# Optimization experiments

Hardware: AMD Instinct MI355X
Metric: run time of the kernel (lower is better)

The kernel has to match this reference:

```python
import jax, jax.numpy as jnp
import numpy as np

B, T, C, H = 2, 2048, 1024, 16
D = C // H  # head dim = 64

def setup_inputs() -> dict:
    key = jax.random.key(0)
    k1, k2, k3 = jax.random.split(key, 3)
    x = jax.random.normal(k1, (B, T, C), dtype=jnp.float32)
    w_attn = jax.random.normal(k2, (C, 3 * C), dtype=jnp.float32) * (1.0 / np.sqrt(C))
    w_proj = jax.random.normal(k3, (C, C), dtype=jnp.float32) * (1.0 / np.sqrt(C))
    return {"x": x, "w_attn": w_attn, "w_proj": w_proj}

def reference(x, w_attn, w_proj):
    # qkv projection: [B,T,3C]
    qkv = jnp.einsum('btc,cd->btd', x, w_attn)
    q, k, v = jnp.split(qkv, 3, axis=-1)
    # reshape to [B,H,T,D]
    q = q.reshape(B, T, H, D).transpose(0, 2, 1, 3)
    k = k.reshape(B, T, H, D).transpose(0, 2, 1, 3)
    v = v.reshape(B, T, H, D).transpose(0, 2, 1, 3)
    scale = 1.0 / jnp.sqrt(jnp.asarray(D, dtype=q.dtype))
    att = jnp.einsum('bhqd,bhkd->bhqk', q, k) * scale  # [B,H,T,T]
    att = jax.nn.softmax(att, axis=-1)
    y = jnp.einsum('bhqk,bhkd->bhqd', att, v)  # [B,H,T,D]
    y = y.transpose(0, 2, 1, 3).reshape(B, T, C)
    return jnp.einsum('btc,cd->btd', y, w_proj)
```

## Files before the change

kernel.cpp:

```cpp
#include <hip/hip_runtime.h>
#include <hip/hip_bf16.h>


typedef unsigned short u16;
using bf16x8 = __attribute__((ext_vector_type(8))) short;
using f32x4  = __attribute__((ext_vector_type(4))) float;

#define T_SEQ 2048
#define CDIM  1024

#define QSCALE 0.18033688011112042f

#if __has_builtin(__builtin_amdgcn_exp2f)
#define EXP2(x) __builtin_amdgcn_exp2f(x)
#else
#define EXP2(x) __expf((x) * 0.6931471805599453f)
#endif

__device__ inline u16 f2bf(float f) {
  __hip_bfloat16 h = __float2bfloat16(f);
  return *reinterpret_cast<u16*>(&h);
}

__device__ inline void gload_lds16(const u16* g, u16* l) {
  __builtin_amdgcn_global_load_lds((const __attribute__((address_space(1))) void*)g,
                                   (__attribute__((address_space(3))) void*)l, 16, 0, 0);
}

__device__ inline int swz128(int r, int c) {
  return (((r << 7) + (c << 1)) ^ ((r & 7) << 4)) >> 1;
}

__global__ __launch_bounds__(256) void conv_bf16_kernel(const float* __restrict__ in,
                                                        u16* __restrict__ out, int n4) {
  int idx = blockIdx.x * 256 + threadIdx.x;
  if (idx >= n4) return;
  float4 v = reinterpret_cast<const float4*>(in)[idx];
  ushort4 o;
  o.x = f2bf(v.x); o.y = f2bf(v.y); o.z = f2bf(v.z); o.w = f2bf(v.w);
  reinterpret_cast<ushort4*>(out)[idx] = o;
}

__global__ __launch_bounds__(256) void transp_conv_kernel(const float* __restrict__ in,
                                                          u16* __restrict__ out, int R, int N,
                                                          int scale_rows, float scale) {
  __shared__ float tile[32][33];
  int nbx = N >> 5;
  int bx = blockIdx.x % nbx, by = blockIdx.x / nbx;
  int tx = threadIdx.x & 31, ty = threadIdx.x >> 5;
#pragma unroll
  for (int rr = ty; rr < 32; rr += 8)
    tile[rr][tx] = in[(long)(by * 32 + rr) * N + bx * 32 + tx];
  __syncthreads();
#pragma unroll
  for (int rr = ty; rr < 32; rr += 8) {
    float s = (bx * 32 + rr) < scale_rows ? scale : 1.0f;
    out[(long)(bx * 32 + rr) * R + by * 32 + tx] = f2bf(tile[tx][rr] * s);
  }
}

template <bool OUT_F32>
__global__ __launch_bounds__(256) void gemm_bt_kernel(const u16* __restrict__ A,
                                                      const u16* __restrict__ Bt,
                                                      void* __restrict__ C,
                                                      int N, int K) {
  __shared__ u16 As[2][128 * 32];
  __shared__ u16 Bs[2][128 * 32];
  const int tid = threadIdx.x;
  const int lane = tid & 63, wid = tid >> 6;
  const int l16 = lane & 15, lh = lane >> 4;
  const int wm = wid >> 1, wn = wid & 1;
  const int tm = blockIdx.x & 31;
  const int tn = blockIdx.x >> 5;

  f32x4 acc[4][4];
#pragma unroll
  for (int i = 0; i < 4; ++i)
#pragma unroll
    for (int j = 0; j < 4; ++j)
      acc[i][j] = f32x4{0.f, 0.f, 0.f, 0.f};

  const long aRow = (long)(tm * 128 + wid * 16 + (lane >> 2)) * K + (lane & 3) * 8;
  const long bRow = (long)(tn * 128 + wid * 16 + (lane >> 2)) * K + (lane & 3) * 8;
  const long rstep = (long)64 * K;
  const int ldsOff = wid * 512;

  gload_lds16(A + aRow, As[0] + ldsOff);
  gload_lds16(A + aRow + rstep, As[0] + ldsOff + 2048);
  gload_lds16(Bt + bRow, Bs[0] + ldsOff);
  gload_lds16(Bt + bRow + rstep, Bs[0] + ldsOff + 2048);
  __syncthreads();

  int cur = 0;
  for (int k0 = 0; k0 < K; k0 += 32) {
    if (k0 + 32 < K) {
      gload_lds16(A + aRow + k0 + 32, As[cur ^ 1] + ldsOff);
      gload_lds16(A + aRow + rstep + k0 + 32, As[cur ^ 1] + ldsOff + 2048);
      gload_lds16(Bt + bRow + k0 + 32, Bs[cur ^ 1] + ldsOff);
      gload_lds16(Bt + bRow + rstep + k0 + 32, Bs[cur ^ 1] + ldsOff + 2048);
    }
    bf16x8 af[4], bfr[4];
#pragma unroll
    for (int i = 0; i < 4; ++i)
      af[i] = *reinterpret_cast<const bf16x8*>(&As[cur][(wm * 64 + i * 16 + l16) * 32 + lh * 8]);
#pragma unroll
    for (int j = 0; j < 4; ++j)
      bfr[j] = *reinterpret_cast<const bf16x8*>(&Bs[cur][(wn * 64 + j * 16 + l16) * 32 + lh * 8]);
#pragma unroll
    for (int i = 0; i < 4; ++i)
#pragma unroll
      for (int j = 0; j < 4; ++j)
        acc[i][j] = __builtin_amdgcn_mfma_f32_16x16x32_bf16(af[i], bfr[j], acc[i][j], 0, 0, 0);
    __syncthreads();
    cur ^= 1;
  }

#pragma unroll
  for (int i = 0; i < 4; ++i) {
#pragma unroll
    for (int j = 0; j < 4; ++j) {
#pragma unroll
      for (int r = 0; r < 4; ++r) {
        long row = tm * 128 + wm * 64 + i * 16 + lh * 4 + r;
        long col = tn * 128 + wn * 64 + j * 16 + l16;
        if (OUT_F32)
          reinterpret_cast<float*>(C)[row * N + col] = acc[i][j][r];
        else
          reinterpret_cast<u16*>(C)[row * N + col] = f2bf(acc[i][j][r]);
      }
    }
  }
}

__global__ __launch_bounds__(256) void vtrans_kernel(const u16* __restrict__ qkv,
                                                     u16* __restrict__ vT) {
  __shared__ u16 Ts[64 * 64];
  const int tid = threadIdx.x;
  const int bid = blockIdx.x;
  const int tt = bid & 31, bh = bid >> 5;
  const int b = bh >> 4, h = bh & 15;
  const int sr = tid >> 2, sc = (tid & 3) * 16;
  const u16* src = qkv + (long)(b * T_SEQ + tt * 64 + sr) * 3072 + 2 * CDIM + h * 64 + sc;
  uint4 v0 = *reinterpret_cast<const uint4*>(src);
  uint4 v1 = *reinterpret_cast<const uint4*>(src + 8);
  *reinterpret_cast<uint4*>(&Ts[swz128(sr, sc)]) = v0;
  *reinterpret_cast<uint4*>(&Ts[swz128(sr, sc + 8)]) = v1;
  __syncthreads();
  union { uint4 u[2]; u16 s[16]; } o;
#pragma unroll
  for (int i = 0; i < 16; ++i) o.s[i] = Ts[swz128(sc + i, sr)];
  u16* dst = vT + (long)(bh * 64 + sr) * T_SEQ + tt * 64 + sc;
  reinterpret_cast<uint4*>(dst)[0] = o.u[0];
  reinterpret_cast<uint4*>(dst)[1] = o.u[1];
}

__global__ __launch_bounds__(256) void attn_kernel(const u16* __restrict__ qkv,
                                                   const u16* __restrict__ vT,
                                                   u16* __restrict__ y) {
  __shared__ u16 Qs[64 * 64];
  __shared__ u16 Ks[64 * 64];
  __shared__ u16 Vt[64 * 64];
  __shared__ u16 Ps[4][16 * 64];
  const int tid = threadIdx.x;
  const int lane = tid & 63, wid = tid >> 6;
  const int l16 = lane & 15, lh = lane >> 4;
  const int bid = blockIdx.x;
  const int qt = bid & 31, h = (bid >> 5) & 15, b = bid >> 9;

  const u16* qbase = qkv + (long)(b * T_SEQ + qt * 64) * 3072 + h * 64;
  const u16* kbase = qkv + (long)(b * T_SEQ) * 3072 + CDIM + h * 64;
  const u16* vtbase = vT + (long)((b * 16 + h) * 64) * T_SEQ;

  const int sr = tid >> 2, sc = (tid & 3) * 16;
  const int ss0 = swz128(sr, sc), ss1 = swz128(sr, sc + 8);

  int kvo[2][4], pwo[4][4];
#pragma unroll
  for (int cb = 0; cb < 4; ++cb) {
    kvo[0][cb] = swz128(cb * 16 + l16, lh * 8);
    kvo[1][cb] = swz128(cb * 16 + l16, 32 + lh * 8);
#pragma unroll
    for (int r = 0; r < 4; ++r) pwo[cb][r] = swz128(lh * 4 + r, cb * 16 + l16);
  }
  const int pro0 = swz128(l16, lh * 8), pro1 = swz128(l16, 32 + lh * 8);

  {
    uint4 v0 = *reinterpret_cast<const uint4*>(qbase + (long)sr * 3072 + sc);
    uint4 v1 = *reinterpret_cast<const uint4*>(qbase + (long)sr * 3072 + sc + 8);
    *reinterpret_cast<uint4*>(&Qs[ss0]) = v0;
    *reinterpret_cast<uint4*>(&Qs[ss1]) = v1;
  }
  uint4 kr0 = *reinterpret_cast<const uint4*>(kbase + (long)sr * 3072 + sc);
  uint4 kr1 = *reinterpret_cast<const uint4*>(kbase + (long)sr * 3072 + sc + 8);
  uint4 vr0 = *reinterpret_cast<const uint4*>(vtbase + (long)sr * T_SEQ + sc);
  uint4 vr1 = *reinterpret_cast<const uint4*>(vtbase + (long)sr * T_SEQ + sc + 8);

  __syncthreads();
  bf16x8 qf0 = *reinterpret_cast<const bf16x8*>(&Qs[swz128(wid * 16 + l16, lh * 8)]);
  bf16x8 qf1 = *reinterpret_cast<const bf16x8*>(&Qs[swz128(wid * 16 + l16, 32 + lh * 8)]);

  f32x4 oacc[4];
  float lp[4] = {0.f, 0.f, 0.f, 0.f};
#pragma unroll
  for (int cb = 0; cb < 4; ++cb) oacc[cb] = f32x4{0.f, 0.f, 0.f, 0.f};

  for (int kt = 0; kt < 32; ++kt) {
    *reinterpret_cast<uint4*>(&Ks[ss0]) = kr0;
    *reinterpret_cast<uint4*>(&Ks[ss1]) = kr1;
    *reinterpret_cast<uint4*>(&Vt[ss0]) = vr0;
    *reinterpret_cast<uint4*>(&Vt[ss1]) = vr1;
    __syncthreads();
    if (kt < 31) {
      const u16* ks = kbase + (long)((kt + 1) * 64 + sr) * 3072 + sc;
      const u16* vs = vtbase + (long)sr * T_SEQ + (kt + 1) * 64 + sc;
      kr0 = *reinterpret_cast<const uint4*>(ks);
      kr1 = *reinterpret_cast<const uint4*>(ks + 8);
      vr0 = *reinterpret_cast<const uint4*>(vs);
      vr1 = *reinterpret_cast<const uint4*>(vs + 8);
    }

    f32x4 sacc[4];
#pragma unroll
    for (int cb = 0; cb < 4; ++cb) {
      sacc[cb] = f32x4{0.f, 0.f, 0.f, 0.f};
      bf16x8 kf0 = *reinterpret_cast<const bf16x8*>(&Ks[kvo[0][cb]]);
      bf16x8 kf1 = *reinterpret_cast<const bf16x8*>(&Ks[kvo[1][cb]]);
      sacc[cb] = __builtin_amdgcn_mfma_f32_16x16x32_bf16(qf0, kf0, sacc[cb], 0, 0, 0);
      sacc[cb] = __builtin_amdgcn_mfma_f32_16x16x32_bf16(qf1, kf1, sacc[cb], 0, 0, 0);
    }

    float p[4][4];
#pragma unroll
    for (int cb = 0; cb < 4; ++cb)
#pragma unroll
      for (int r = 0; r < 4; ++r) p[cb][r] = EXP2(sacc[cb][r]);
#pragma unroll
    for (int r = 0; r < 4; ++r)
      lp[r] += (p[0][r] + p[1][r]) + (p[2][r] + p[3][r]);

#pragma unroll
    for (int cb = 0; cb < 4; ++cb)
#pragma unroll
      for (int r = 0; r < 4; ++r)
        Ps[wid][pwo[cb][r]] = f2bf(p[cb][r]);

    bf16x8 pf0 = *reinterpret_cast<const bf16x8*>(&Ps[wid][pro0]);
    bf16x8 pf1 = *reinterpret_cast<const bf16x8*>(&Ps[wid][pro1]);

#pragma unroll
    for (int cb = 0; cb < 4; ++cb) {
      bf16x8 vf0 = *reinterpret_cast<const bf16x8*>(&Vt[kvo[0][cb]]);
      bf16x8 vf1 = *reinterpret_cast<const bf16x8*>(&Vt[kvo[1][cb]]);
      oacc[cb] = __builtin_amdgcn_mfma_f32_16x16x32_bf16(pf0, vf0, oacc[cb], 0, 0, 0);
      oacc[cb] = __builtin_amdgcn_mfma_f32_16x16x32_bf16(pf1, vf1, oacc[cb], 0, 0, 0);
    }
    __syncthreads();
  }

  float inv[4];
#pragma unroll
  for (int r = 0; r < 4; ++r) {
    float s = lp[r];
    s += __shfl_xor(s, 1);
    s += __shfl_xor(s, 2);
    s += __shfl_xor(s, 4);
    s += __shfl_xor(s, 8);
    inv[r] = __builtin_amdgcn_rcpf(s);
  }
  u16* ybase = y + (long)(b * T_SEQ + qt * 64 + wid * 16) * CDIM + h * 64;
#pragma unroll
  for (int cb = 0; cb < 4; ++cb)
#pragma unroll
    for (int r = 0; r < 4; ++r)
      ybase[(long)(lh * 4 + r) * CDIM + cb * 16 + l16] = f2bf(oacc[cb][r] * inv[r]);
}

extern "C" void kernel_launch(void* const* d_in, const int* in_sizes, int n_in,
                              void* d_out, int out_size, void* d_ws, size_t ws_size,
                              hipStream_t stream) {
  const float* x      = (const float*)d_in[0];
  const float* w_attn = (const float*)d_in[1];
  const float* w_proj = (const float*)d_in[2];

  char* ws = (char*)d_ws;
  u16* xb   = (u16*)(ws + 0);
  u16* wat  = (u16*)(ws + 8388608);
  u16* wpt  = (u16*)(ws + 14680064);
  u16* qkvb = (u16*)(ws + 16777216);
  u16* yb   = (u16*)(ws + 41943040);
  u16* vT   = xb;

  conv_bf16_kernel<<<4096, 256, 0, stream>>>(x, xb, 1048576);
  transp_conv_kernel<<<96 * 32, 256, 0, stream>>>(w_attn, wat, 1024, 3072, 1024, QSCALE);
  transp_conv_kernel<<<32 * 32, 256, 0, stream>>>(w_proj, wpt, 1024, 1024, 0, 1.0f);
  gemm_bt_kernel<false><<<32 * 24, 256, 0, stream>>>(xb, wat, qkvb, 3072, 1024);
  vtrans_kernel<<<32 * 32, 256, 0, stream>>>(qkvb, vT);
  attn_kernel<<<2 * 16 * 32, 256, 0, stream>>>(qkvb, vT, yb);
  gemm_bt_kernel<true><<<32 * 8, 256, 0, stream>>>(yb, wpt, d_out, 1024, 1024);
}
```

Measured before the change: 205.8 us.

## Transpose attention MFMA operands, vectorize P/O LDS stores, remap GEMM block order

Swaps the A/B operands of the attention MFMAs so each lane holds four consecutive key columns of one query row. This allows packed 8-byte bf16 stores of P into LDS with an XOR swizzle, reduces the row-sum to a single scalar with two shuffles, and stages the output through LDS for 16-byte coalesced global stores instead of scalar 2-byte writes. Separately, the GEMM block index is remapped across eight groups so consecutive blocks cover different tile regions, aiming at better cache or XCD locality. It adds an extra LDS round trip in the epilogue and depends on the new swizzle being conflict-free.

```diff
diff --git a/kernel.cpp b/kernel.cpp
--- a/kernel.cpp
+++ b/kernel.cpp
@@ -20,6 +20,9 @@
 __device__ inline u16 f2bf(float f) {
   __hip_bfloat16 h = __float2bfloat16(f);
   return *reinterpret_cast<u16*>(&h);
+}
+__device__ inline unsigned pk2bf(float a, float b) {
+  return (unsigned)f2bf(a) | ((unsigned)f2bf(b) << 16);
 }
 
 __device__ inline void gload_lds16(const u16* g, u16* l) {
@@ -70,8 +73,11 @@
   const int lane = tid & 63, wid = tid >> 6;
   const int l16 = lane & 15, lh = lane >> 4;
   const int wm = wid >> 1, wn = wid & 1;
-  const int tm = blockIdx.x & 31;
-  const int tn = blockIdx.x >> 5;
+  const int q8 = gridDim.x >> 3;
+  const int wg = (blockIdx.x & 7) * q8 + (blockIdx.x >> 3);
+  const int nTn = N >> 7;
+  const int tn = wg % nTn;
+  const int tm = wg / nTn;
 
   f32x4 acc[4][4];
 #pragma unroll
@@ -174,15 +180,18 @@
   const int sr = tid >> 2, sc = (tid & 3) * 16;
   const int ss0 = swz128(sr, sc), ss1 = swz128(sr, sc + 8);
 
-  int kvo[2][4], pwo[4][4];
+  int kvo[2][4];
 #pragma unroll
   for (int cb = 0; cb < 4; ++cb) {
     kvo[0][cb] = swz128(cb * 16 + l16, lh * 8);
     kvo[1][cb] = swz128(cb * 16 + l16, 32 + lh * 8);
-#pragma unroll
-    for (int r = 0; r < 4; ++r) pwo[cb][r] = swz128(lh * 4 + r, cb * 16 + l16);
-  }
-  const int pro0 = swz128(l16, lh * 8), pro1 = swz128(l16, 32 + lh * 8);
+  }
+  const int pxor = (l16 & 7) << 3;
+  int pwi[4];
+#pragma unroll
+  for (int cb = 0; cb < 4; ++cb) pwi[cb] = (l16 * 64 + cb * 16 + lh * 4) ^ pxor;
+  const int pri0 = (l16 * 64 + lh * 8) ^ pxor;
+  const int pri1 = (l16 * 64 + 32 + lh * 8) ^ pxor;
 
   {
     uint4 v0 = *reinterpret_cast<const uint4*>(qbase + (long)sr * 3072 + sc);
@@ -200,7 +209,7 @@
   bf16x8 qf1 = *reinterpret_cast<const bf16x8*>(&Qs[swz128(wid * 16 + l16, 32 + lh * 8)]);
 
   f32x4 oacc[4];
-  float lp[4] = {0.f, 0.f, 0.f, 0.f};
+  float lp = 0.f;
 #pragma unroll
   for (int cb = 0; cb < 4; ++cb) oacc[cb] = f32x4{0.f, 0.f, 0.f, 0.f};
 
@@ -225,8 +234,8 @@
       sacc[cb] = f32x4{0.f, 0.f, 0.f, 0.f};
       bf16x8 kf0 = *reinterpret_cast<const bf16x8*>(&Ks[kvo[0][cb]]);
       bf16x8 kf1 = *reinterpret_cast<const bf16x8*>(&Ks[kvo[1][cb]]);
-      sacc[cb] = __builtin_amdgcn_mfma_f32_16x16x32_bf16(qf0, kf0, sacc[cb], 0, 0, 0);
-      sacc[cb] = __builtin_amdgcn_mfma_f32_16x16x32_bf16(qf1, kf1, sacc[cb], 0, 0, 0);
+      sacc[cb] = __builtin_amdgcn_mfma_f32_16x16x32_bf16(kf0, qf0, sacc[cb], 0, 0, 0);
+      sacc[cb] = __builtin_amdgcn_mfma_f32_16x16x32_bf16(kf1, qf1, sacc[cb], 0, 0, 0);
     }
 
     float p[4][4];
@@ -235,44 +244,50 @@
 #pragma unroll
       for (int r = 0; r < 4; ++r) p[cb][r] = EXP2(sacc[cb][r]);
 #pragma unroll
-    for (int r = 0; r < 4; ++r)
-      lp[r] += (p[0][r] + p[1][r]) + (p[2][r] + p[3][r]);
-
-#pragma unroll
     for (int cb = 0; cb < 4; ++cb)
-#pragma unroll
-      for (int r = 0; r < 4; ++r)
-        Ps[wid][pwo[cb][r]] = f2bf(p[cb][r]);
-
-    bf16x8 pf0 = *reinterpret_cast<const bf16x8*>(&Ps[wid][pro0]);
-    bf16x8 pf1 = *reinterpret_cast<const bf16x8*>(&Ps[wid][pro1]);
+      lp += (p[cb][0] + p[cb][1]) + (p[cb][2] + p[cb][3]);
+#pragma unroll
+    for (int cb = 0; cb < 4; ++cb) {
+      uint2 w2;
+      w2.x = pk2bf(p[cb][0], p[cb][1]);
+      w2.y = pk2bf(p[cb][2], p[cb][3]);
+      *reinterpret_cast<uint2*>(&Ps[wid][pwi[cb]]) = w2;
+    }
+
+    bf16x8 pf0 = *reinterpret_cast<const bf16x8*>(&Ps[wid][pri0]);
+    bf16x8 pf1 = *reinterpret_cast<const bf16x8*>(&Ps[wid][pri1]);
 
 #pragma unroll
     for (int cb = 0; cb < 4; ++cb) {
       bf16x8 vf0 = *reinterpret_cast<const bf16x8*>(&Vt[kvo[0][cb]]);
       bf16x8 vf1 = *reinterpret_cast<const bf16x8*>(&Vt[kvo[1][cb]]);
-      oacc[cb] = __builtin_amdgcn_mfma_f32_16x16x32_bf16(pf0, vf0, oacc[cb], 0, 0, 0);
-      oacc[cb] = __builtin_amdgcn_mfma_f32_16x16x32_bf16(pf1, vf1, oacc[cb], 0, 0, 0);
+      oacc[cb] = __builtin_amdgcn_mfma_f32_16x16x32_bf16(vf0, pf0, oacc[cb], 0, 0, 0);
+      oacc[cb] = __builtin_amdgcn_mfma_f32_16x16x32_bf16(vf1, pf1, oacc[cb], 0, 0, 0);
     }
     __syncthreads();
   }
 
-  float inv[4];
-#pragma unroll
-  for (int r = 0; r < 4; ++r) {
-    float s = lp[r];
-    s += __shfl_xor(s, 1);
-    s += __shfl_xor(s, 2);
-    s += __shfl_xor(s, 4);
-    s += __shfl_xor(s, 8);
-    inv[r] = __builtin_amdgcn_rcpf(s);
-  }
-  u16* ybase = y + (long)(b * T_SEQ + qt * 64 + wid * 16) * CDIM + h * 64;
-#pragma unroll
-  for (int cb = 0; cb < 4; ++cb)
-#pragma unroll
-    for (int r = 0; r < 4; ++r)
-      ybase[(long)(lh * 4 + r) * CDIM + cb * 16 + l16] = f2bf(oacc[cb][r] * inv[r]);
+  float s = lp;
+  s += __shfl_xor(s, 16);
+  s += __shfl_xor(s, 32);
+  const float inv = __builtin_amdgcn_rcpf(s);
+
+#pragma unroll
+  for (int cb = 0; cb < 4; ++cb) {
+    uint2 w2;
+    w2.x = pk2bf(oacc[cb][0] * inv, oacc[cb][1] * inv);
+    w2.y = pk2bf(oacc[cb][2] * inv, oacc[cb][3] * inv);
+    *reinterpret_cast<uint2*>(&Ps[wid][pwi[cb]]) = w2;
+  }
+  const int er = lane >> 2, ec = lane & 3;
+  const int exr = (er & 7) << 3;
+  const int eri0 = (er * 64 + ec * 16) ^ exr;
+  const int eri1 = (er * 64 + ec * 16 + 8) ^ exr;
+  uint4 o0 = *reinterpret_cast<const uint4*>(&Ps[wid][eri0]);
+  uint4 o1 = *reinterpret_cast<const uint4*>(&Ps[wid][eri1]);
+  u16* yrow = y + (long)(b * T_SEQ + qt * 64 + wid * 16 + er) * CDIM + h * 64 + ec * 16;
+  reinterpret_cast<uint4*>(yrow)[0] = o0;
+  *reinterpret_cast<uint4*>(yrow + 8) = o1;
 }
 
 extern "C" void kernel_launch(void* const* d_in, const int* in_sizes, int n_in,
```

Result: no change. 207.0 us (+0.6%).
